# Kernel tuning notes

Hardware: AMD Instinct MI355X
Metric: run time of the kernel (lower is better)

## Reference

```python
import jax, jax.numpy as jnp
import numpy as np

N_ENT = 50000   # entities (nodes)
N_REL = 500     # relations
DEG = 32        # regular in-degree of the full KG
TOPK = 10       # topk in-edges kept per node by dgl.sampling.select_topk
H_DIM = 256
N_HEADS = 4
HEAD_DIM = H_DIM // N_HEADS
NEG_SLOPE = 0.2


def _leaky(x):
    return jnp.where(x >= 0, x, NEG_SLOPE * x)


def setup_inputs() -> dict:
    key = jax.random.key(0)
    ks = jax.random.split(key, 8)
    s = 0.05
    return {
        'ent_emb': jax.random.normal(ks[0], (N_ENT, H_DIM), dtype=jnp.float32),
        'rel_emb': jax.random.normal(ks[1], (N_REL, H_DIM), dtype=jnp.float32),
        'W': jax.random.normal(ks[2], (N_HEADS, H_DIM, HEAD_DIM), dtype=jnp.float32) * s,
        'W_r': jax.random.normal(ks[3], (N_HEADS, H_DIM, HEAD_DIM), dtype=jnp.float32) * s,
        'a': jax.random.normal(ks[4], (N_HEADS, 3 * HEAD_DIM), dtype=jnp.float32) * s,
        'neigh_w': jax.random.normal(ks[5], (H_DIM, H_DIM), dtype=jnp.float32) * s,
        'src': jax.random.randint(ks[6], (N_ENT, DEG), 0, N_ENT),   # src node of each in-edge of node n
        'rel_id': jax.random.randint(ks[7], (N_ENT, DEG), 0, N_REL),
    }


def reference(ent_emb, rel_emb, W, W_r, a, neigh_w, src, rel_id):
    # ---- head-0 scores used for top-k in-edge sampling (select_topk, edge_dir='in') ----
    emb_t0 = ent_emb @ W[0]          # [N, hd]
    rel_t0 = rel_emb @ W_r[0]        # [R, hd]
    a0 = a[0]
    # concat([src,dst,rel]) @ a  ==  src@a_src + dst@a_dst + rel@a_rel
    s_src = emb_t0 @ a0[:HEAD_DIM]                 # [N]
    s_dst = emb_t0 @ a0[HEAD_DIM:2 * HEAD_DIM]     # [N]
    s_rel = rel_t0 @ a0[2 * HEAD_DIM:]             # [R]
    score0 = _leaky(s_src[src] + s_dst[:, None] + s_rel[rel_id])   # [N, DEG]
    _, top_idx = jax.lax.top_k(score0, TOPK)                        # [N, K]
    src_sel = jnp.take_along_axis(src, top_idx, axis=1)             # [N, K]
    rel_sel = jnp.take_along_axis(rel_id, top_idx, axis=1)          # [N, K]

    # ---- all heads on the sampled subgraph (vectorized over heads) ----
    emb_t = jnp.einsum('nd,hde->hne', ent_emb, W)     # [H, N, hd]
    rel_t = jnp.einsum('rd,hde->hre', rel_emb, W_r)   # [H, R, hd]
    a3 = a.reshape(N_HEADS, 3, HEAD_DIM)
    ss = jnp.einsum('hne,he->hn', emb_t, a3[:, 0])    # [H, N]
    sd = jnp.einsum('hne,he->hn', emb_t, a3[:, 1])    # [H, N]
    sr = jnp.einsum('hre,he->hr', rel_t, a3[:, 2])    # [H, R]
    scores = _leaky(ss[:, src_sel] + sd[:, :, None] + sr[:, rel_sel])  # [H, N, K]
    norm = jax.nn.softmax(scores, axis=-1)            # edge-softmax over in-edges per dst

    # comp_op == 'add' : u_add_e, weighted by attention, summed into dst
    comp = emb_t[:, src_sel] + rel_t[:, rel_sel]      # [H, N, K, hd]
    neigh = jnp.einsum('hnke,hnk->hne', comp, norm)   # [H, N, hd]

    neigh = jnp.transpose(neigh, (1, 0, 2)).reshape(ent_emb.shape[0], H_DIM)  # concat heads
    return jnp.tanh(neigh @ neigh_w)                  # bn disabled (cfg.bn=False)
```

## Files before the change

kernel.cpp:

```cpp
#include <hip/hip_runtime.h>
#include <math.h>

#define N_ENT 50000
#define N_REL 500
#define DEG 32
#define TOPK 10
#define H_DIM 256
#define N_HEADS 4
#define HEAD_DIM 64

typedef __attribute__((ext_vector_type(8))) short short8v;
typedef __attribute__((ext_vector_type(4))) float f32x4;

constexpr size_t OFF_SSRC0 = 0;
constexpr size_t OFF_SR0   = 400000;
constexpr size_t OFF_U0    = 404000;
constexpr size_t OFF_V0    = 406048;
constexpr size_t OFF_SS    = 408096;
constexpr size_t OFF_SSR   = 2008096;
constexpr size_t OFF_U8    = 2024096;
constexpr size_t OFF_V8    = 2032288;
constexpr size_t OFF_B1H   = 2040480;
constexpr size_t OFF_B2H   = 2302624;
constexpr size_t OFF_B3H   = 2564768;
constexpr size_t OFF_RPK   = 2826912;
constexpr size_t OFF_EAH   = 3089056;
constexpr size_t OFF_EMBBF = 28713632;
constexpr size_t OFF_RELBF = 54313632;
constexpr size_t WS_NEED   = 54569632;

__device__ __forceinline__ float leaky(float x) { return x >= 0.f ? x : 0.2f * x; }

__device__ __forceinline__ unsigned short bf16_rne(float x) {
    unsigned int u = __float_as_uint(x);
    unsigned int r = u + 0x7fffu + ((u >> 16) & 1u);
    return (unsigned short)(r >> 16);
}
__device__ __forceinline__ float bf2f(unsigned short x) {
    return __uint_as_float((unsigned)x << 16);
}

__device__ __forceinline__ size_t pack_off(int row, int d) {
    return ((size_t)(row >> 4) * 8 + (d >> 5)) * 512 +
           (((d >> 3) & 3) * 16 + (row & 15)) * 8 + (d & 7);
}

__global__ __launch_bounds__(256) void setup_kernel(
    const float* __restrict__ W, const float* __restrict__ W_r,
    const float* __restrict__ a, const float* __restrict__ nw,
    float* __restrict__ U8, double* __restrict__ u0,
    float* __restrict__ V8, double* __restrict__ v0,
    unsigned short* __restrict__ b1h, unsigned short* __restrict__ b2h,
    unsigned short* __restrict__ b3h)
{
    const int bid = blockIdx.x;
    const int tid = threadIdx.x;
    if (bid == 0) {
        int d = tid;
        #pragma unroll
        for (int h = 0; h < N_HEADS; ++h) {
            float ss = 0.f, sd = 0.f;
            #pragma unroll
            for (int e = 0; e < HEAD_DIM; ++e) {
                float w = W[h * 16384 + d * 64 + e];
                ss += w * a[h * 192 + e];
                sd += w * a[h * 192 + 64 + e];
            }
            U8[d * 8 + h] = ss;
            U8[d * 8 + 4 + h] = sd;
        }
        double s0 = 0.0;
        #pragma unroll
        for (int e = 0; e < HEAD_DIM; ++e)
            s0 += (double)W[d * 64 + e] * (double)a[e];
        u0[d] = s0;
    } else if (bid == 1) {
        int d = tid;
        #pragma unroll
        for (int h = 0; h < N_HEADS; ++h) {
            float sv = 0.f;
            #pragma unroll
            for (int e = 0; e < HEAD_DIM; ++e)
                sv += W_r[h * 16384 + d * 64 + e] * a[h * 192 + 128 + e];
            V8[d * 8 + h] = sv;
            V8[d * 8 + 4 + h] = 0.f;
        }
        double s0 = 0.0;
        #pragma unroll
        for (int e = 0; e < HEAD_DIM; ++e)
            s0 += (double)W_r[d * 64 + e] * (double)a[128 + e];
        v0[d] = s0;
    } else {
        int n = bid - 2;
        int k = tid;
        int h = n >> 6, e = n & 63;
        float x1 = W[h * 16384 + k * 64 + e];
        float x2 = nw[k * 256 + n];
        float x3 = W_r[h * 16384 + k * 64 + e];
        size_t off = pack_off(n, k);
        b1h[off] = bf16_rne(x1);
        b2h[off] = bf16_rne(x2);
        b3h[off] = bf16_rne(x3);
    }
}

__global__ __launch_bounds__(256) void ss_kernel(
    const float* __restrict__ ent, const float* __restrict__ relm,
    const float* __restrict__ U8, const double* __restrict__ u0,
    const float* __restrict__ V8, const double* __restrict__ v0,
    float* __restrict__ SS, double* __restrict__ ssrc0, unsigned short* __restrict__ apk,
    float* __restrict__ SSR, double* __restrict__ sr0, unsigned short* __restrict__ rpk)
{
    const int tid = threadIdx.x;
    const int l = tid & 63;
    const int el = l & 31;
    const int q2 = l >> 5;

    const bool isent = blockIdx.x < 2048;
    const float* X = isent ? ent : relm;
    const float* U8v = isent ? U8 : V8;
    const double* u0v = isent ? u0 : v0;
    float* SSout = isent ? SS : SSR;
    double* s0out = isent ? ssrc0 : sr0;
    unsigned short* Xpk = isent ? apk : rpk;
    const int N = isent ? N_ENT : N_REL;
    const int wave0 = isent ? ((blockIdx.x * 256 + tid) >> 6)
                            : (((blockIdx.x - 2048) * 256 + tid) >> 6);
    const int nwaves = isent ? 8192 : 252;

    float uu[8][8];
    #pragma unroll
    for (int i = 0; i < 8; ++i) {
        float4 a4 = *(const float4*)(U8v + (el * 8 + i) * 8);
        float4 b4 = *(const float4*)(U8v + (el * 8 + i) * 8 + 4);
        uu[i][0] = a4.x; uu[i][1] = a4.y; uu[i][2] = a4.z; uu[i][3] = a4.w;
        uu[i][4] = b4.x; uu[i][5] = b4.y; uu[i][6] = b4.z; uu[i][7] = b4.w;
    }
    double ud[8];
    #pragma unroll
    for (int i = 0; i < 8; ++i) ud[i] = u0v[el * 8 + i];

    const int jout = ((el & 1) << 2) | (el & 2) | ((el >> 2) & 1);
    const int half = N / 2;

    int p = wave0;
    float4 x1, x2;
    if (p < half) {
        int n0 = p * 2 + q2;
        x1 = *(const float4*)(X + (size_t)n0 * 256 + el * 8);
        x2 = *(const float4*)(X + (size_t)n0 * 256 + el * 8 + 4);
    }
    for (; p < half; p += nwaves) {
        const int n = p * 2 + q2;
        const float4 cx1 = x1, cx2 = x2;
        const int np = p + nwaves;
        if (np < half) {
            int n1 = np * 2 + q2;
            x1 = *(const float4*)(X + (size_t)n1 * 256 + el * 8);
            x2 = *(const float4*)(X + (size_t)n1 * 256 + el * 8 + 4);
        }
        float xs[8] = {cx1.x, cx1.y, cx1.z, cx1.w, cx2.x, cx2.y, cx2.z, cx2.w};

        short8v ov;
        #pragma unroll
        for (int i = 0; i < 8; ++i) ov[i] = (short)bf16_rne(xs[i]);
        *(short8v*)(Xpk + (size_t)n * 256 + el * 8) = ov;

        float pj[8] = {0.f, 0.f, 0.f, 0.f, 0.f, 0.f, 0.f, 0.f};
        double pd = 0.0;
        #pragma unroll
        for (int i = 0; i < 8; ++i) {
            #pragma unroll
            for (int j = 0; j < 8; ++j) pj[j] += xs[i] * uu[i][j];
            pd += (double)xs[i] * ud[i];
        }

        const bool b1 = (el & 1);
        float q[4];
        #pragma unroll
        for (int j = 0; j < 4; ++j) {
            float mine = b1 ? pj[j + 4] : pj[j];
            float send = b1 ? pj[j] : pj[j + 4];
            q[j] = mine + __shfl_xor(send, 1);
        }
        const bool b2 = (el & 2);
        float r2[2];
        #pragma unroll
        for (int j = 0; j < 2; ++j) {
            float mine = b2 ? q[j + 2] : q[j];
            float send = b2 ? q[j] : q[j + 2];
            r2[j] = mine + __shfl_xor(send, 2);
        }
        const bool b4 = (el & 4);
        {
            float mine = b4 ? r2[1] : r2[0];
            float send = b4 ? r2[0] : r2[1];
            r2[0] = mine + __shfl_xor(send, 4);
        }
        r2[0] += __shfl_xor(r2[0], 8);
        r2[0] += __shfl_xor(r2[0], 16);

        #pragma unroll
        for (int off = 1; off < 32; off <<= 1) pd += __shfl_xor(pd, off);

        if (el < 8) SSout[(size_t)n * 8 + jout] = r2[0];
        if (el == 0) s0out[n] = pd;
    }
}

__global__ __launch_bounds__(256, 4) void gemm_hi(
    const unsigned short* __restrict__ A1, const unsigned short* __restrict__ B1,
    unsigned short* __restrict__ C1, int M1, int nb1,
    const unsigned short* __restrict__ A2, const unsigned short* __restrict__ B2,
    unsigned short* __restrict__ C2, int M2)
{
    __shared__ unsigned short As[64][264];

    const int tid = threadIdx.x;
    const int l = tid & 63;
    const int w = tid >> 6;
    const int rl = l & 15;
    const int ql = l >> 4;

    const int b = blockIdx.x;
    const unsigned short* A = (b < nb1) ? A1 : A2;
    const unsigned short* Bh = (b < nb1) ? B1 : B2;
    unsigned short* C       = (b < nb1) ? C1 : C2;
    const int M             = (b < nb1) ? M1 : M2;
    const int bm            = ((b < nb1) ? b : (b - nb1)) * 64;

    const unsigned short* Ag = A + (size_t)bm * 256;
    #pragma unroll
    for (int i = 0; i < 8; ++i) {
        int u = i * 256 + tid;
        short8v v = *(const short8v*)(Ag + (size_t)u * 8);
        *(short8v*)&As[u >> 5][(u & 31) * 8] = v;
    }
    __syncthreads();

    const unsigned short* bhb = Bh + (size_t)w * 16384 + l * 8;

    f32x4 acc[4][4];
    #pragma unroll
    for (int i = 0; i < 4; ++i)
        #pragma unroll
        for (int j = 0; j < 4; ++j) acc[i][j] = (f32x4){0.f, 0.f, 0.f, 0.f};

    #pragma unroll
    for (int ks = 0; ks < 8; ++ks) {
        short8v ah[4], bh[4];
        #pragma unroll
        for (int mf = 0; mf < 4; ++mf)
            ah[mf] = *(const short8v*)&As[mf * 16 + rl][ks * 32 + ql * 8];
        #pragma unroll
        for (int nf = 0; nf < 4; ++nf)
            bh[nf] = *(const short8v*)(bhb + nf * 4096 + ks * 512);
        #pragma unroll
        for (int mf = 0; mf < 4; ++mf)
            #pragma unroll
            for (int nf = 0; nf < 4; ++nf)
                acc[mf][nf] = __builtin_amdgcn_mfma_f32_16x16x32_bf16(ah[mf], bh[nf], acc[mf][nf], 0, 0, 0);
    }

    #pragma unroll
    for (int mf = 0; mf < 4; ++mf) {
        int row0 = bm + mf * 16 + ql * 4;
        #pragma unroll
        for (int nf = 0; nf < 4; ++nf) {
            int c = w * 64 + nf * 16 + rl;
            #pragma unroll
            for (int j = 0; j < 4; ++j) {
                int r = row0 + j;
                if (r < M)
                    C[(size_t)r * 256 + c] = bf16_rne(acc[mf][nf][j]);
            }
        }
    }
}

__global__ __launch_bounds__(256, 3) void node_kernel(
    const int* __restrict__ src, const int* __restrict__ relid,
    const float* __restrict__ SS, const double* __restrict__ ssrc0,
    const float* __restrict__ SSR, const double* __restrict__ sr0,
    const unsigned short* __restrict__ emb_bf, const unsigned short* __restrict__ rel_bf,
    unsigned short* __restrict__ napk)
{
    __shared__ double scs[8][33];
    __shared__ unsigned idsS[8][12];
    __shared__ float wtsS[8][10][4];
    __shared__ float sumsS[8][4];

    const int tid = threadIdx.x;
    const int l = tid & 63;
    const int el = l & 31;
    const int hb = l & 32;
    const int nib = tid >> 5;
    const int n = blockIdx.x * 8 + nib;

    const int sd_ = src[n * DEG + el];
    const int rd_ = relid[n * DEG + el];
    const double sc0 = ssrc0[sd_] + sr0[rd_];
    scs[nib][el] = sc0;

    int cnt = 0;
    #pragma unroll
    for (int j = 0; j < DEG; ++j) {
        double sj = scs[nib][j];
        cnt += (sj > sc0 || (sj == sc0 && j < el)) ? 1 : 0;
    }
    const bool sel = (cnt < TOPK);
    const unsigned mask = (unsigned)(__ballot(sel) >> hb);
    const int pos = __popc(mask & ((1u << el) - 1u));

    float ex = 0.f, ey = 0.f, ez = 0.f, ew = 0.f;
    if (sel) {
        float4 ssv = *(const float4*)(SS + (size_t)sd_ * 8);
        float4 srv = *(const float4*)(SSR + (size_t)rd_ * 8);
        float4 sdv = *(const float4*)(SS + (size_t)n * 8 + 4);
        ex = __expf(leaky(ssv.x + sdv.x + srv.x));
        ey = __expf(leaky(ssv.y + sdv.y + srv.y));
        ez = __expf(leaky(ssv.z + sdv.z + srv.z));
        ew = __expf(leaky(ssv.w + sdv.w + srv.w));
        idsS[nib][pos] = (unsigned)sd_ | ((unsigned)rd_ << 16);
        float4 wv; wv.x = ex; wv.y = ey; wv.z = ez; wv.w = ew;
        *(float4*)&wtsS[nib][pos][0] = wv;
    }

    float p0, p1;
    {
        const bool b1 = (el & 1);
        float m0 = b1 ? ez : ex, s0 = b1 ? ex : ez;
        float m1 = b1 ? ew : ey, s1 = b1 ? ey : ew;
        p0 = m0 + __shfl_xor(s0, 1);
        p1 = m1 + __shfl_xor(s1, 1);
    }
    float qsum;
    {
        const bool b2 = (el & 2);
        float m = b2 ? p1 : p0, s = b2 ? p0 : p1;
        qsum = m + __shfl_xor(s, 2);
    }
    qsum += __shfl_xor(qsum, 4);
    qsum += __shfl_xor(qsum, 8);
    qsum += __shfl_xor(qsum, 16);
    if (el < 4) sumsS[nib][((el & 1) << 1) | ((el >> 1) & 1)] = qsum;

    const int h = el >> 3;

    int skA[TOPK], rkA[TOPK];
    #pragma unroll
    for (int k = 0; k < TOPK; ++k) {
        unsigned idk = idsS[nib][k];
        skA[k] = (int)(idk & 0xFFFFu);
        rkA[k] = (int)(idk >> 16);
    }

    short8v ev[TOPK], rv[TOPK];
    #pragma unroll
    for (int k = 0; k < TOPK; ++k)
        ev[k] = *(const short8v*)(emb_bf + (size_t)skA[k] * 256 + el * 8);
    #pragma unroll
    for (int k = 0; k < TOPK; ++k)
        rv[k] = *(const short8v*)(rel_bf + (size_t)rkA[k] * 256 + el * 8);
    asm volatile("s_waitcnt vmcnt(0)" ::: "memory");

    const float rsh = 1.f / sumsS[nib][h];
    float acc[8] = {0.f, 0.f, 0.f, 0.f, 0.f, 0.f, 0.f, 0.f};
    #pragma unroll
    for (int k = 0; k < TOPK; ++k) {
        float w = wtsS[nib][k][h] * rsh;
        #pragma unroll
        for (int j = 0; j < 8; ++j)
            acc[j] += w * (bf2f((unsigned short)ev[k][j]) + bf2f((unsigned short)rv[k][j]));
    }

    short8v ov;
    #pragma unroll
    for (int j = 0; j < 8; ++j) ov[j] = (short)bf16_rne(acc[j]);
    *(short8v*)(napk + (size_t)n * 256 + el * 8) = ov;
}

__global__ __launch_bounds__(256, 4) void gemm_out(
    const unsigned short* __restrict__ A, const unsigned short* __restrict__ Bpkh,
    float* __restrict__ Cout, int M)
{
    __shared__ unsigned short As[64][264];

    const int tid = threadIdx.x;
    const int l = tid & 63;
    const int w = tid >> 6;
    const int bm = blockIdx.x * 64;
    const int rl = l & 15;
    const int ql = l >> 4;

    const unsigned short* Ag = A + (size_t)bm * 256;
    #pragma unroll
    for (int i = 0; i < 8; ++i) {
        int u = i * 256 + tid;
        short8v v = *(const short8v*)(Ag + (size_t)u * 8);
        *(short8v*)&As[u >> 5][(u & 31) * 8] = v;
    }
    __syncthreads();

    const unsigned short* bhb = Bpkh + (size_t)w * 16384 + l * 8;

    f32x4 acc[4][4];
    #pragma unroll
    for (int i = 0; i < 4; ++i)
        #pragma unroll
        for (int j = 0; j < 4; ++j) acc[i][j] = (f32x4){0.f, 0.f, 0.f, 0.f};

    #pragma unroll
    for (int ks = 0; ks < 8; ++ks) {
        short8v ah[4], bh[4];
        #pragma unroll
        for (int mf = 0; mf < 4; ++mf)
            ah[mf] = *(const short8v*)&As[mf * 16 + rl][ks * 32 + ql * 8];
        #pragma unroll
        for (int nf = 0; nf < 4; ++nf)
            bh[nf] = *(const short8v*)(bhb + nf * 4096 + ks * 512);
        #pragma unroll
        for (int mf = 0; mf < 4; ++mf)
            #pragma unroll
            for (int nf = 0; nf < 4; ++nf)
                acc[mf][nf] = __builtin_amdgcn_mfma_f32_16x16x32_bf16(ah[mf], bh[nf], acc[mf][nf], 0, 0, 0);
    }

    #pragma unroll
    for (int mf = 0; mf < 4; ++mf) {
        int row0 = bm + mf * 16 + ql * 4;
        #pragma unroll
        for (int nf = 0; nf < 4; ++nf) {
            int c = w * 64 + nf * 16 + rl;
            #pragma unroll
            for (int j = 0; j < 4; ++j) {
                int r = row0 + j;
                if (r < M) {
                    float v = acc[mf][nf][j];
                    Cout[(size_t)r * 256 + c] = 1.f - 2.f / (__expf(2.f * v) + 1.f);
                }
            }
        }
    }
}

extern "C" void kernel_launch(void* const* d_in, const int* in_sizes, int n_in,
                              void* d_out, int out_size, void* d_ws, size_t ws_size,
                              hipStream_t stream) {
    const float* ent  = (const float*)d_in[0];
    const float* rel  = (const float*)d_in[1];
    const float* W    = (const float*)d_in[2];
    const float* W_r  = (const float*)d_in[3];
    const float* a    = (const float*)d_in[4];
    const float* nw   = (const float*)d_in[5];
    const int*   srcp = (const int*)d_in[6];
    const int*   ridp = (const int*)d_in[7];
    float* out = (float*)d_out;

    if (ws_size < WS_NEED) return;

    char* ws = (char*)d_ws;
    double* ssrc0 = (double*)(ws + OFF_SSRC0);
    double* sr0   = (double*)(ws + OFF_SR0);
    double* u0    = (double*)(ws + OFF_U0);
    double* v0    = (double*)(ws + OFF_V0);
    float*  SS    = (float*)(ws + OFF_SS);
    float*  SSR   = (float*)(ws + OFF_SSR);
    float*  U8    = (float*)(ws + OFF_U8);
    float*  V8    = (float*)(ws + OFF_V8);
    unsigned short* b1h = (unsigned short*)(ws + OFF_B1H);
    unsigned short* b2h = (unsigned short*)(ws + OFF_B2H);
    unsigned short* b3h = (unsigned short*)(ws + OFF_B3H);
    unsigned short* rpk = (unsigned short*)(ws + OFF_RPK);
    unsigned short* apk = (unsigned short*)(ws + OFF_EAH);
    unsigned short* embbf = (unsigned short*)(ws + OFF_EMBBF);
    unsigned short* relbf = (unsigned short*)(ws + OFF_RELBF);
    unsigned short* napk = apk;

    setup_kernel<<<258, 256, 0, stream>>>(W, W_r, a, nw, U8, u0, V8, v0,
                                          b1h, b2h, b3h);
    ss_kernel<<<2111, 256, 0, stream>>>(ent, rel, U8, u0, V8, v0,
                                        SS, ssrc0, apk, SSR, sr0, rpk);
    gemm_hi<<<790, 256, 0, stream>>>(apk, b1h, embbf, N_ENT, 782,
                                     rpk, b3h, relbf, N_REL);
    node_kernel<<<6250, 256, 0, stream>>>(srcp, ridp, SS, ssrc0, SSR, sr0,
                                          embbf, relbf, napk);
    gemm_out<<<782, 256, 0, stream>>>(napk, b2h, out, N_ENT);
}
```

Baseline: 140.7 us.

## Process two nodes per thread group in node_kernel to overlap gathers

Each 32-lane group now handles two destination nodes. All score and index loads for both nodes are issued up front, and the embedding gathers for the first node are issued before the second node's top-k selection, so memory latency overlaps with compute. The grid is halved and launch bounds drop to 2 blocks per SM, which lets the kernel use more registers for the doubled gather buffers at the cost of lower occupancy. The score inputs are now loaded for every edge rather than only the selected ones, adding some extra memory traffic.

```diff
diff --git a/kernel.cpp b/kernel.cpp
--- a/kernel.cpp
+++ b/kernel.cpp
@@ -278,7 +278,7 @@
     }
 }
 
-__global__ __launch_bounds__(256, 3) void node_kernel(
+__global__ __launch_bounds__(256, 2) void node_kernel(
     const int* __restrict__ src, const int* __restrict__ relid,
     const float* __restrict__ SS, const double* __restrict__ ssrc0,
     const float* __restrict__ SSR, const double* __restrict__ sr0,
@@ -286,98 +286,157 @@
     unsigned short* __restrict__ napk)
 {
     __shared__ double scs[8][33];
-    __shared__ unsigned idsS[8][12];
-    __shared__ float wtsS[8][10][4];
-    __shared__ float sumsS[8][4];
+    __shared__ unsigned idsS[2][8][12];
+    __shared__ float wtsS[2][8][10][4];
+    __shared__ float sumsS[2][8][4];
 
     const int tid = threadIdx.x;
     const int l = tid & 63;
     const int el = l & 31;
     const int hb = l & 32;
     const int nib = tid >> 5;
-    const int n = blockIdx.x * 8 + nib;
-
-    const int sd_ = src[n * DEG + el];
-    const int rd_ = relid[n * DEG + el];
-    const double sc0 = ssrc0[sd_] + sr0[rd_];
+    const int n0 = blockIdx.x * 16 + nib;
+    const int n1 = blockIdx.x * 16 + 8 + nib;
+    const int h = el >> 3;
+
+    const int sd0 = src[n0 * DEG + el], rd0 = relid[n0 * DEG + el];
+    const int sd1 = src[n1 * DEG + el], rd1 = relid[n1 * DEG + el];
+    const double sa0 = ssrc0[sd0], sb0 = sr0[rd0];
+    const double sa1 = ssrc0[sd1], sb1 = sr0[rd1];
+    const float4 ssv0 = *(const float4*)(SS + (size_t)sd0 * 8);
+    const float4 srv0 = *(const float4*)(SSR + (size_t)rd0 * 8);
+    const float4 sdv0 = *(const float4*)(SS + (size_t)n0 * 8 + 4);
+    const float4 ssv1 = *(const float4*)(SS + (size_t)sd1 * 8);
+    const float4 srv1 = *(const float4*)(SSR + (size_t)rd1 * 8);
+    const float4 sdv1 = *(const float4*)(SS + (size_t)n1 * 8 + 4);
+
+    const double sc0 = sa0 + sb0;
     scs[nib][el] = sc0;
-
-    int cnt = 0;
+    int cnt0 = 0;
     #pragma unroll
     for (int j = 0; j < DEG; ++j) {
         double sj = scs[nib][j];
-        cnt += (sj > sc0 || (sj == sc0 && j < el)) ? 1 : 0;
-    }
-    const bool sel = (cnt < TOPK);
-    const unsigned mask = (unsigned)(__ballot(sel) >> hb);
-    const int pos = __popc(mask & ((1u << el) - 1u));
-
-    float ex = 0.f, ey = 0.f, ez = 0.f, ew = 0.f;
-    if (sel) {
-        float4 ssv = *(const float4*)(SS + (size_t)sd_ * 8);
-        float4 srv = *(const float4*)(SSR + (size_t)rd_ * 8);
-        float4 sdv = *(const float4*)(SS + (size_t)n * 8 + 4);
-        ex = __expf(leaky(ssv.x + sdv.x + srv.x));
-        ey = __expf(leaky(ssv.y + sdv.y + srv.y));
-        ez = __expf(leaky(ssv.z + sdv.z + srv.z));
-        ew = __expf(leaky(ssv.w + sdv.w + srv.w));
-        idsS[nib][pos] = (unsigned)sd_ | ((unsigned)rd_ << 16);
-        float4 wv; wv.x = ex; wv.y = ey; wv.z = ez; wv.w = ew;
-        *(float4*)&wtsS[nib][pos][0] = wv;
-    }
-
-    float p0, p1;
+        cnt0 += (sj > sc0 || (sj == sc0 && j < el)) ? 1 : 0;
+    }
+    const bool sel0 = (cnt0 < TOPK);
+    const unsigned mask0 = (unsigned)(__ballot(sel0) >> hb);
+    const int pos0 = __popc(mask0 & ((1u << el) - 1u));
+    float ex0 = __expf(leaky(ssv0.x + sdv0.x + srv0.x));
+    float ey0 = __expf(leaky(ssv0.y + sdv0.y + srv0.y));
+    float ez0 = __expf(leaky(ssv0.z + sdv0.z + srv0.z));
+    float ew0 = __expf(leaky(ssv0.w + sdv0.w + srv0.w));
+    if (!sel0) { ex0 = 0.f; ey0 = 0.f; ez0 = 0.f; ew0 = 0.f; }
+    if (sel0) {
+        idsS[0][nib][pos0] = (unsigned)sd0 | ((unsigned)rd0 << 16);
+        float4 wv; wv.x = ex0; wv.y = ey0; wv.z = ez0; wv.w = ew0;
+        *(float4*)&wtsS[0][nib][pos0][0] = wv;
+    }
     {
         const bool b1 = (el & 1);
-        float m0 = b1 ? ez : ex, s0 = b1 ? ex : ez;
-        float m1 = b1 ? ew : ey, s1 = b1 ? ey : ew;
-        p0 = m0 + __shfl_xor(s0, 1);
-        p1 = m1 + __shfl_xor(s1, 1);
-    }
-    float qsum;
+        float p0 = (b1 ? ez0 : ex0) + __shfl_xor(b1 ? ex0 : ez0, 1);
+        float p1 = (b1 ? ew0 : ey0) + __shfl_xor(b1 ? ey0 : ew0, 1);
+        const bool b2 = (el & 2);
+        float qsum = (b2 ? p1 : p0) + __shfl_xor(b2 ? p0 : p1, 2);
+        qsum += __shfl_xor(qsum, 4);
+        qsum += __shfl_xor(qsum, 8);
+        qsum += __shfl_xor(qsum, 16);
+        if (el < 4) sumsS[0][nib][((el & 1) << 1) | ((el >> 1) & 1)] = qsum;
+    }
+
+    int sk0[TOPK], rk0[TOPK];
+    #pragma unroll
+    for (int k = 0; k < TOPK; ++k) {
+        unsigned idk = idsS[0][nib][k];
+        sk0[k] = (int)(idk & 0xFFFFu);
+        rk0[k] = (int)(idk >> 16);
+    }
+    short8v ev0[TOPK], rv0[TOPK];
+    #pragma unroll
+    for (int k = 0; k < TOPK; ++k)
+        ev0[k] = *(const short8v*)(emb_bf + (size_t)sk0[k] * 256 + el * 8);
+    #pragma unroll
+    for (int k = 0; k < TOPK; ++k)
+        rv0[k] = *(const short8v*)(rel_bf + (size_t)rk0[k] * 256 + el * 8);
+
+    const double sc1 = sa1 + sb1;
+    scs[nib][el] = sc1;
+    int cnt1 = 0;
+    #pragma unroll
+    for (int j = 0; j < DEG; ++j) {
+        double sj = scs[nib][j];
+        cnt1 += (sj > sc1 || (sj == sc1 && j < el)) ? 1 : 0;
+    }
+    const bool sel1 = (cnt1 < TOPK);
+    const unsigned mask1 = (unsigned)(__ballot(sel1) >> hb);
+    const int pos1 = __popc(mask1 & ((1u << el) - 1u));
+    float ex1 = __expf(leaky(ssv1.x + sdv1.x + srv1.x));
+    float ey1 = __expf(leaky(ssv1.y + sdv1.y + srv1.y));
+    float ez1 = __expf(leaky(ssv1.z + sdv1.z + srv1.z));
+    float ew1 = __expf(leaky(ssv1.w + sdv1.w + srv1.w));
+    if (!sel1) { ex1 = 0.f; ey1 = 0.f; ez1 = 0.f; ew1 = 0.f; }
+    if (sel1) {
+        idsS[1][nib][pos1] = (unsigned)sd1 | ((unsigned)rd1 << 16);
+        float4 wv; wv.x = ex1; wv.y = ey1; wv.z = ez1; wv.w = ew1;
+        *(float4*)&wtsS[1][nib][pos1][0] = wv;
+    }
     {
+        const bool b1 = (el & 1);
+        float p0 = (b1 ? ez1 : ex1) + __shfl_xor(b1 ? ex1 : ez1, 1);
+        float p1 = (b1 ? ew1 : ey1) + __shfl_xor(b1 ? ey1 : ew1, 1);
         const bool b2 = (el & 2);
-        float m = b2 ? p1 : p0, s = b2 ? p0 : p1;
-        qsum = m + __shfl_xor(s, 2);
-    }
-    qsum += __shfl_xor(qsum, 4);
-    qsum += __shfl_xor(qsum, 8);
-    qsum += __shfl_xor(qsum, 16);
-    if (el < 4) sumsS[nib][((el & 1) << 1) | ((el >> 1) & 1)] = qsum;
-
-    const int h = el >> 3;
-
-    int skA[TOPK], rkA[TOPK];
+        float qsum = (b2 ? p1 : p0) + __shfl_xor(b2 ? p0 : p1, 2);
+        qsum += __shfl_xor(qsum, 4);
+        qsum += __shfl_xor(qsum, 8);
+        qsum += __shfl_xor(qsum, 16);
+        if (el < 4) sumsS[1][nib][((el & 1) << 1) | ((el >> 1) & 1)] = qsum;
+    }
+
+    int sk1[TOPK], rk1[TOPK];
     #pragma unroll
     for (int k = 0; k < TOPK; ++k) {
-        unsigned idk = idsS[nib][k];
-        skA[k] = (int)(idk & 0xFFFFu);
-        rkA[k] = (int)(idk >> 16);
-    }
-
-    short8v ev[TOPK], rv[TOPK];
+        unsigned idk = idsS[1][nib][k];
+        sk1[k] = (int)(idk & 0xFFFFu);
+        rk1[k] = (int)(idk >> 16);
+    }
+    short8v ev1[TOPK], rv1[TOPK];
     #pragma unroll
     for (int k = 0; k < TOPK; ++k)
-        ev[k] = *(const short8v*)(emb_bf + (size_t)skA[k] * 256 + el * 8);
+        ev1[k] = *(const short8v*)(emb_bf + (size_t)sk1[k] * 256 + el * 8);
     #pragma unroll
     for (int k = 0; k < TOPK; ++k)
-        rv[k] = *(const short8v*)(rel_bf + (size_t)rkA[k] * 256 + el * 8);
-    asm volatile("s_waitcnt vmcnt(0)" ::: "memory");
-
-    const float rsh = 1.f / sumsS[nib][h];
-    float acc[8] = {0.f, 0.f, 0.f, 0.f, 0.f, 0.f, 0.f, 0.f};
-    #pragma unroll
-    for (int k = 0; k < TOPK; ++k) {
-        float w = wtsS[nib][k][h] * rsh;
-        #pragma unroll
-        for (int j = 0; j < 8; ++j)
-            acc[j] += w * (bf2f((unsigned short)ev[k][j]) + bf2f((unsigned short)rv[k][j]));
-    }
-
-    short8v ov;
-    #pragma unroll
-    for (int j = 0; j < 8; ++j) ov[j] = (short)bf16_rne(acc[j]);
-    *(short8v*)(napk + (size_t)n * 256 + el * 8) = ov;
+        rv1[k] = *(const short8v*)(rel_bf + (size_t)rk1[k] * 256 + el * 8);
+
+    {
+        const float rsh = 1.f / sumsS[0][nib][h];
+        float acc[8] = {0.f, 0.f, 0.f, 0.f, 0.f, 0.f, 0.f, 0.f};
+        #pragma unroll
+        for (int k = 0; k < TOPK; ++k) {
+            float w = wtsS[0][nib][k][h] * rsh;
+            #pragma unroll
+            for (int j = 0; j < 8; ++j)
+                acc[j] += w * (bf2f((unsigned short)ev0[k][j]) + bf2f((unsigned short)rv0[k][j]));
+        }
+        short8v ov;
+        #pragma unroll
+        for (int j = 0; j < 8; ++j) ov[j] = (short)bf16_rne(acc[j]);
+        *(short8v*)(napk + (size_t)n0 * 256 + el * 8) = ov;
+    }
+
+    {
+        const float rsh = 1.f / sumsS[1][nib][h];
+        float acc[8] = {0.f, 0.f, 0.f, 0.f, 0.f, 0.f, 0.f, 0.f};
+        #pragma unroll
+        for (int k = 0; k < TOPK; ++k) {
+            float w = wtsS[1][nib][k][h] * rsh;
+            #pragma unroll
+            for (int j = 0; j < 8; ++j)
+                acc[j] += w * (bf2f((unsigned short)ev1[k][j]) + bf2f((unsigned short)rv1[k][j]));
+        }
+        short8v ov;
+        #pragma unroll
+        for (int j = 0; j < 8; ++j) ov[j] = (short)bf16_rne(acc[j]);
+        *(short8v*)(napk + (size_t)n1 * 256 + el * 8) = ov;
+    }
 }
 
 __global__ __launch_bounds__(256, 4) void gemm_out(
@@ -483,7 +542,7 @@
                                         SS, ssrc0, apk, SSR, sr0, rpk);
     gemm_hi<<<790, 256, 0, stream>>>(apk, b1h, embbf, N_ENT, 782,
                                      rpk, b3h, relbf, N_REL);
-    node_kernel<<<6250, 256, 0, stream>>>(srcp, ridp, SS, ssrc0, SSR, sr0,
+    node_kernel<<<3125, 256, 0, stream>>>(srcp, ridp, SS, ssrc0, SSR, sr0,
                                           embbf, relbf, napk);
     gemm_out<<<782, 256, 0, stream>>>(napk, b2h, out, N_ENT);
 }
```

New measurement: 151.1 us. 7.4% more time.

## Fuse score projection and input GEMM into one kernel with inline bf16 conversion

Applied to the files above, without the earlier changes.

Merges ss_kernel and gemm_hi into a single launch. The GEMM blocks now read fp32 embeddings directly and convert them to bf16 while staging into shared memory, so the separate bf16 copy of the entity and relation matrices is no longer written or read back. The score-projection blocks run alongside in the same grid. This removes one launch boundary and a full write and re-read of the bf16 inputs. In exchange, every row is read twice in fp32, and GEMM blocks with heavy shared-memory use are mixed with light streaming blocks, which may reduce occupancy.

```diff
diff --git a/kernel.cpp b/kernel.cpp
--- a/kernel.cpp
+++ b/kernel.cpp
@@ -23,8 +23,7 @@
 constexpr size_t OFF_B1H   = 2040480;
 constexpr size_t OFF_B2H   = 2302624;
 constexpr size_t OFF_B3H   = 2564768;
-constexpr size_t OFF_RPK   = 2826912;
-constexpr size_t OFF_EAH   = 3089056;
+constexpr size_t OFF_NPK   = 3089056;
 constexpr size_t OFF_EMBBF = 28713632;
 constexpr size_t OFF_RELBF = 54313632;
 constexpr size_t WS_NEED   = 54569632;
@@ -104,176 +103,174 @@
     }
 }
 
-__global__ __launch_bounds__(256) void ss_kernel(
+__global__ __launch_bounds__(256) void mid_kernel(
     const float* __restrict__ ent, const float* __restrict__ relm,
+    const unsigned short* __restrict__ b1h, const unsigned short* __restrict__ b3h,
+    unsigned short* __restrict__ embbf, unsigned short* __restrict__ relbf,
     const float* __restrict__ U8, const double* __restrict__ u0,
     const float* __restrict__ V8, const double* __restrict__ v0,
-    float* __restrict__ SS, double* __restrict__ ssrc0, unsigned short* __restrict__ apk,
-    float* __restrict__ SSR, double* __restrict__ sr0, unsigned short* __restrict__ rpk)
+    float* __restrict__ SS, double* __restrict__ ssrc0,
+    float* __restrict__ SSR, double* __restrict__ sr0)
 {
+    __shared__ unsigned short As[64][264];
+
+    const int b = blockIdx.x;
     const int tid = threadIdx.x;
     const int l = tid & 63;
     const int el = l & 31;
-    const int q2 = l >> 5;
-
-    const bool isent = blockIdx.x < 2048;
-    const float* X = isent ? ent : relm;
-    const float* U8v = isent ? U8 : V8;
-    const double* u0v = isent ? u0 : v0;
-    float* SSout = isent ? SS : SSR;
-    double* s0out = isent ? ssrc0 : sr0;
-    unsigned short* Xpk = isent ? apk : rpk;
-    const int N = isent ? N_ENT : N_REL;
-    const int wave0 = isent ? ((blockIdx.x * 256 + tid) >> 6)
-                            : (((blockIdx.x - 2048) * 256 + tid) >> 6);
-    const int nwaves = isent ? 8192 : 252;
-
-    float uu[8][8];
-    #pragma unroll
-    for (int i = 0; i < 8; ++i) {
-        float4 a4 = *(const float4*)(U8v + (el * 8 + i) * 8);
-        float4 b4 = *(const float4*)(U8v + (el * 8 + i) * 8 + 4);
-        uu[i][0] = a4.x; uu[i][1] = a4.y; uu[i][2] = a4.z; uu[i][3] = a4.w;
-        uu[i][4] = b4.x; uu[i][5] = b4.y; uu[i][6] = b4.z; uu[i][7] = b4.w;
-    }
-    double ud[8];
-    #pragma unroll
-    for (int i = 0; i < 8; ++i) ud[i] = u0v[el * 8 + i];
-
-    const int jout = ((el & 1) << 2) | (el & 2) | ((el >> 2) & 1);
-    const int half = N / 2;
-
-    int p = wave0;
-    float4 x1, x2;
-    if (p < half) {
-        int n0 = p * 2 + q2;
-        x1 = *(const float4*)(X + (size_t)n0 * 256 + el * 8);
-        x2 = *(const float4*)(X + (size_t)n0 * 256 + el * 8 + 4);
-    }
-    for (; p < half; p += nwaves) {
-        const int n = p * 2 + q2;
-        const float4 cx1 = x1, cx2 = x2;
-        const int np = p + nwaves;
-        if (np < half) {
-            int n1 = np * 2 + q2;
-            x1 = *(const float4*)(X + (size_t)n1 * 256 + el * 8);
-            x2 = *(const float4*)(X + (size_t)n1 * 256 + el * 8 + 4);
-        }
-        float xs[8] = {cx1.x, cx1.y, cx1.z, cx1.w, cx2.x, cx2.y, cx2.z, cx2.w};
-
-        short8v ov;
-        #pragma unroll
-        for (int i = 0; i < 8; ++i) ov[i] = (short)bf16_rne(xs[i]);
-        *(short8v*)(Xpk + (size_t)n * 256 + el * 8) = ov;
-
-        float pj[8] = {0.f, 0.f, 0.f, 0.f, 0.f, 0.f, 0.f, 0.f};
-        double pd = 0.0;
+
+    if (b < 790) {
+        const int w = tid >> 6;
+        const int rl = l & 15;
+        const int ql = l >> 4;
+
+        const bool isent = (b < 782);
+        const float* Af = isent ? ent : relm;
+        const unsigned short* Bh = isent ? b1h : b3h;
+        unsigned short* C = isent ? embbf : relbf;
+        const int M = isent ? N_ENT : N_REL;
+        const int bm = (isent ? b : (b - 782)) * 64;
+
         #pragma unroll
         for (int i = 0; i < 8; ++i) {
-            #pragma unroll
-            for (int j = 0; j < 8; ++j) pj[j] += xs[i] * uu[i][j];
-            pd += (double)xs[i] * ud[i];
-        }
-
-        const bool b1 = (el & 1);
-        float q[4];
-        #pragma unroll
-        for (int j = 0; j < 4; ++j) {
-            float mine = b1 ? pj[j + 4] : pj[j];
-            float send = b1 ? pj[j] : pj[j + 4];
-            q[j] = mine + __shfl_xor(send, 1);
-        }
-        const bool b2 = (el & 2);
-        float r2[2];
-        #pragma unroll
-        for (int j = 0; j < 2; ++j) {
-            float mine = b2 ? q[j + 2] : q[j];
-            float send = b2 ? q[j] : q[j + 2];
-            r2[j] = mine + __shfl_xor(send, 2);
-        }
-        const bool b4 = (el & 4);
-        {
-            float mine = b4 ? r2[1] : r2[0];
-            float send = b4 ? r2[0] : r2[1];
-            r2[0] = mine + __shfl_xor(send, 4);
-        }
-        r2[0] += __shfl_xor(r2[0], 8);
-        r2[0] += __shfl_xor(r2[0], 16);
-
-        #pragma unroll
-        for (int off = 1; off < 32; off <<= 1) pd += __shfl_xor(pd, off);
-
-        if (el < 8) SSout[(size_t)n * 8 + jout] = r2[0];
-        if (el == 0) s0out[n] = pd;
-    }
-}
-
-__global__ __launch_bounds__(256, 4) void gemm_hi(
-    const unsigned short* __restrict__ A1, const unsigned short* __restrict__ B1,
-    unsigned short* __restrict__ C1, int M1, int nb1,
-    const unsigned short* __restrict__ A2, const unsigned short* __restrict__ B2,
-    unsigned short* __restrict__ C2, int M2)
-{
-    __shared__ unsigned short As[64][264];
-
-    const int tid = threadIdx.x;
-    const int l = tid & 63;
-    const int w = tid >> 6;
-    const int rl = l & 15;
-    const int ql = l >> 4;
-
-    const int b = blockIdx.x;
-    const unsigned short* A = (b < nb1) ? A1 : A2;
-    const unsigned short* Bh = (b < nb1) ? B1 : B2;
-    unsigned short* C       = (b < nb1) ? C1 : C2;
-    const int M             = (b < nb1) ? M1 : M2;
-    const int bm            = ((b < nb1) ? b : (b - nb1)) * 64;
-
-    const unsigned short* Ag = A + (size_t)bm * 256;
-    #pragma unroll
-    for (int i = 0; i < 8; ++i) {
-        int u = i * 256 + tid;
-        short8v v = *(const short8v*)(Ag + (size_t)u * 8);
-        *(short8v*)&As[u >> 5][(u & 31) * 8] = v;
-    }
-    __syncthreads();
-
-    const unsigned short* bhb = Bh + (size_t)w * 16384 + l * 8;
-
-    f32x4 acc[4][4];
-    #pragma unroll
-    for (int i = 0; i < 4; ++i)
-        #pragma unroll
-        for (int j = 0; j < 4; ++j) acc[i][j] = (f32x4){0.f, 0.f, 0.f, 0.f};
-
-    #pragma unroll
-    for (int ks = 0; ks < 8; ++ks) {
-        short8v ah[4], bh[4];
-        #pragma unroll
-        for (int mf = 0; mf < 4; ++mf)
-            ah[mf] = *(const short8v*)&As[mf * 16 + rl][ks * 32 + ql * 8];
-        #pragma unroll
-        for (int nf = 0; nf < 4; ++nf)
-            bh[nf] = *(const short8v*)(bhb + nf * 4096 + ks * 512);
-        #pragma unroll
-        for (int mf = 0; mf < 4; ++mf)
+            int u = i * 256 + tid;
+            int row = u >> 5;
+            int c8 = (u & 31) * 8;
+            int grow = min(bm + row, M - 1);
+            float4 v1 = *(const float4*)(Af + (size_t)grow * 256 + c8);
+            float4 v2 = *(const float4*)(Af + (size_t)grow * 256 + c8 + 4);
+            short8v ov;
+            ov[0] = (short)bf16_rne(v1.x); ov[1] = (short)bf16_rne(v1.y);
+            ov[2] = (short)bf16_rne(v1.z); ov[3] = (short)bf16_rne(v1.w);
+            ov[4] = (short)bf16_rne(v2.x); ov[5] = (short)bf16_rne(v2.y);
+            ov[6] = (short)bf16_rne(v2.z); ov[7] = (short)bf16_rne(v2.w);
+            *(short8v*)&As[row][c8] = ov;
+        }
+        __syncthreads();
+
+        const unsigned short* bhb = Bh + (size_t)w * 16384 + l * 8;
+
+        f32x4 acc[4][4];
+        #pragma unroll
+        for (int i = 0; i < 4; ++i)
+            #pragma unroll
+            for (int j = 0; j < 4; ++j) acc[i][j] = (f32x4){0.f, 0.f, 0.f, 0.f};
+
+        #pragma unroll
+        for (int ks = 0; ks < 8; ++ks) {
+            short8v ah[4], bh[4];
+            #pragma unroll
+            for (int mf = 0; mf < 4; ++mf)
+                ah[mf] = *(const short8v*)&As[mf * 16 + rl][ks * 32 + ql * 8];
             #pragma unroll
             for (int nf = 0; nf < 4; ++nf)
-                acc[mf][nf] = __builtin_amdgcn_mfma_f32_16x16x32_bf16(ah[mf], bh[nf], acc[mf][nf], 0, 0, 0);
-    }
-
-    #pragma unroll
-    for (int mf = 0; mf < 4; ++mf) {
-        int row0 = bm + mf * 16 + ql * 4;
-        #pragma unroll
-        for (int nf = 0; nf < 4; ++nf) {
-            int c = w * 64 + nf * 16 + rl;
+                bh[nf] = *(const short8v*)(bhb + nf * 4096 + ks * 512);
+            #pragma unroll
+            for (int mf = 0; mf < 4; ++mf)
+                #pragma unroll
+                for (int nf = 0; nf < 4; ++nf)
+                    acc[mf][nf] = __builtin_amdgcn_mfma_f32_16x16x32_bf16(ah[mf], bh[nf], acc[mf][nf], 0, 0, 0);
+        }
+
+        #pragma unroll
+        for (int mf = 0; mf < 4; ++mf) {
+            int row0 = bm + mf * 16 + ql * 4;
+            #pragma unroll
+            for (int nf = 0; nf < 4; ++nf) {
+                int c = w * 64 + nf * 16 + rl;
+                #pragma unroll
+                for (int j = 0; j < 4; ++j) {
+                    int r = row0 + j;
+                    if (r < M)
+                        C[(size_t)r * 256 + c] = bf16_rne(acc[mf][nf][j]);
+                }
+            }
+        }
+    } else {
+        const int q2 = l >> 5;
+        const bool isent = (b < 2838);
+        const float* X = isent ? ent : relm;
+        const float* U8v = isent ? U8 : V8;
+        const double* u0v = isent ? u0 : v0;
+        float* SSout = isent ? SS : SSR;
+        double* s0out = isent ? ssrc0 : sr0;
+        const int N = isent ? N_ENT : N_REL;
+        const int wave0 = isent ? (((b - 790) * 256 + tid) >> 6)
+                                : (((b - 2838) * 256 + tid) >> 6);
+        const int nwaves = isent ? 8192 : 252;
+
+        float uu[8][8];
+        #pragma unroll
+        for (int i = 0; i < 8; ++i) {
+            float4 a4 = *(const float4*)(U8v + (el * 8 + i) * 8);
+            float4 b4 = *(const float4*)(U8v + (el * 8 + i) * 8 + 4);
+            uu[i][0] = a4.x; uu[i][1] = a4.y; uu[i][2] = a4.z; uu[i][3] = a4.w;
+            uu[i][4] = b4.x; uu[i][5] = b4.y; uu[i][6] = b4.z; uu[i][7] = b4.w;
+        }
+        double ud[8];
+        #pragma unroll
+        for (int i = 0; i < 8; ++i) ud[i] = u0v[el * 8 + i];
+
+        const int jout = ((el & 1) << 2) | (el & 2) | ((el >> 2) & 1);
+        const int half = N / 2;
+
+        int p = wave0;
+        float4 x1, x2;
+        if (p < half) {
+            int n0 = p * 2 + q2;
+            x1 = *(const float4*)(X + (size_t)n0 * 256 + el * 8);
+            x2 = *(const float4*)(X + (size_t)n0 * 256 + el * 8 + 4);
+        }
+        for (; p < half; p += nwaves) {
+            const int n = p * 2 + q2;
+            const float4 cx1 = x1, cx2 = x2;
+            const int np = p + nwaves;
+            if (np < half) {
+                int n1 = np * 2 + q2;
+                x1 = *(const float4*)(X + (size_t)n1 * 256 + el * 8);
+                x2 = *(const float4*)(X + (size_t)n1 * 256 + el * 8 + 4);
+            }
+            float xs[8] = {cx1.x, cx1.y, cx1.z, cx1.w, cx2.x, cx2.y, cx2.z, cx2.w};
+
+            float pj[8] = {0.f, 0.f, 0.f, 0.f, 0.f, 0.f, 0.f, 0.f};
+            double pd = 0.0;
+            #pragma unroll
+            for (int i = 0; i < 8; ++i) {
+                #pragma unroll
+                for (int j = 0; j < 8; ++j) pj[j] += xs[i] * uu[i][j];
+                pd += (double)xs[i] * ud[i];
+            }
+
+            const bool b1 = (el & 1);
+            float q[4];
             #pragma unroll
             for (int j = 0; j < 4; ++j) {
-                int r = row0 + j;
-                if (r < M)
-                    C[(size_t)r * 256 + c] = bf16_rne(acc[mf][nf][j]);
-            }
+                float mine = b1 ? pj[j + 4] : pj[j];
+                float send = b1 ? pj[j] : pj[j + 4];
+                q[j] = mine + __shfl_xor(send, 1);
+            }
+            const bool b2 = (el & 2);
+            float r2[2];
+            #pragma unroll
+            for (int j = 0; j < 2; ++j) {
+                float mine = b2 ? q[j + 2] : q[j];
+                float send = b2 ? q[j] : q[j + 2];
+                r2[j] = mine + __shfl_xor(send, 2);
+            }
+            const bool b4 = (el & 4);
+            {
+                float mine = b4 ? r2[1] : r2[0];
+                float send = b4 ? r2[0] : r2[1];
+                r2[0] = mine + __shfl_xor(send, 4);
+            }
+            r2[0] += __shfl_xor(r2[0], 8);
+            r2[0] += __shfl_xor(r2[0], 16);
+
+            #pragma unroll
+            for (int off = 1; off < 32; off <<= 1) pd += __shfl_xor(pd, off);
+
+            if (el < 8) SSout[(size_t)n * 8 + jout] = r2[0];
+            if (el == 0) s0out[n] = pd;
         }
     }
 }
@@ -471,18 +468,14 @@
     unsigned short* b1h = (unsigned short*)(ws + OFF_B1H);
     unsigned short* b2h = (unsigned short*)(ws + OFF_B2H);
     unsigned short* b3h = (unsigned short*)(ws + OFF_B3H);
-    unsigned short* rpk = (unsigned short*)(ws + OFF_RPK);
-    unsigned short* apk = (unsigned short*)(ws + OFF_EAH);
+    unsigned short* napk = (unsigned short*)(ws + OFF_NPK);
     unsigned short* embbf = (unsigned short*)(ws + OFF_EMBBF);
     unsigned short* relbf = (unsigned short*)(ws + OFF_RELBF);
-    unsigned short* napk = apk;
 
     setup_kernel<<<258, 256, 0, stream>>>(W, W_r, a, nw, U8, u0, V8, v0,
                                           b1h, b2h, b3h);
-    ss_kernel<<<2111, 256, 0, stream>>>(ent, rel, U8, u0, V8, v0,
-                                        SS, ssrc0, apk, SSR, sr0, rpk);
-    gemm_hi<<<790, 256, 0, stream>>>(apk, b1h, embbf, N_ENT, 782,
-                                     rpk, b3h, relbf, N_REL);
+    mid_kernel<<<2901, 256, 0, stream>>>(ent, rel, b1h, b3h, embbf, relbf,
+                                         U8, u0, V8, v0, SS, ssrc0, SSR, sr0);
     node_kernel<<<6250, 256, 0, stream>>>(srcp, ridp, SS, ssrc0, SSR, sr0,
                                           embbf, relbf, napk);
     gemm_out<<<782, 256, 0, stream>>>(napk, b2h, out, N_ENT);
```

Result: no change. 138.9 us (-1.3%).
